# Optimization experiments

Hardware: AMD Instinct MI355X
Metric: run time of the kernel (lower is better)

## Reference

```python
import jax, jax.numpy as jnp
import numpy as np

B, L, V, H = 4096, 80, 256, 512  # batch, NLE_TERM_CO, charset, msg_hdim


def setup_inputs() -> dict:
    key = jax.random.key(0)
    k0, k1, k2 = jax.random.split(key, 3)
    message = jax.random.randint(k0, (B, L), 0, V, dtype=jnp.int64)
    # Linear(i_dim=L*V, H): store weight as [L*V, H] (i.e. torch weight.T)
    W1 = jax.random.normal(k1, (L * V, H), dtype=jnp.float32) * 0.01
    b1 = jnp.zeros((H,), dtype=jnp.float32)
    W2 = jax.random.normal(k2, (H, H), dtype=jnp.float32) * 0.02
    b2 = jnp.zeros((H,), dtype=jnp.float32)
    return {"message": message, "W1": W1, "b1": b1, "W2": W2, "b2": b2}


def reference(message, W1, b1, W2, b2):
    # one_hot(message, 256).reshape(B, L*256) @ W1  ==  gather rows of W1 at
    # flat index pos*256 + char, summed over positions (no one-hot materialized).
    idx = message + jnp.arange(L, dtype=message.dtype)[None, :] * V  # [B, L]
    emb = jnp.take(W1, idx, axis=0).sum(axis=1)                       # [B, H]
    h = jax.nn.relu(emb + b1)
    out = jax.nn.relu(h @ W2 + b2)
    return out
```

## Files before the change

### kernel.cpp

```cpp
#include <hip/hip_runtime.h>
#include <hip/hip_bf16.h>
#include <stdint.h>

#define B_ 4096
#define L_ 80
#define V_ 256
#define H_ 512

typedef __attribute__((ext_vector_type(4))) float f32x4;
typedef __attribute__((ext_vector_type(8))) short bf16x8;

__global__ __launch_bounds__(256) void w2_transpose(
    const float* __restrict__ W2, __hip_bfloat16* __restrict__ W2T) {
  int i = blockIdx.x * blockDim.x + threadIdx.x;
  int n = i >> 9, k = i & 511;
  W2T[i] = __float2bfloat16(W2[k * H_ + n]);
}

__global__ __launch_bounds__(512) void encode_gather(
    const int* __restrict__ msg, const float* __restrict__ W1,
    const float* __restrict__ b1, __hip_bfloat16* __restrict__ h) {
  const int BT = 16;
  __shared__ int offs[BT * L_];
  const int t = threadIdx.x;
  const int b0 = blockIdx.x * BT;

  for (int i = t; i < BT * L_; i += 512) {
    int b = i / L_, l = i - b * L_;
    offs[i] = (l * V_ + msg[(b0 + b) * L_ + l]) * H_;
  }
  __syncthreads();

  float acc[BT];
#pragma unroll
  for (int b = 0; b < BT; ++b) acc[b] = 0.f;

  for (int l = 0; l < L_; ++l) {
#pragma unroll
    for (int b = 0; b < BT; ++b) {
      acc[b] += W1[offs[b * L_ + l] + t];
    }
  }

  const float bias = b1[t];
#pragma unroll
  for (int b = 0; b < BT; ++b) {
    float v = acc[b] + bias;
    v = v > 0.f ? v : 0.f;
    h[(size_t)(b0 + b) * H_ + t] = __float2bfloat16(v);
  }
}

__global__ __launch_bounds__(256) void gemm_out(
    const __hip_bfloat16* __restrict__ h, const __hip_bfloat16* __restrict__ W2T,
    const float* __restrict__ b2, float* __restrict__ out) {
  const int wid = threadIdx.x >> 6;
  const int lane = threadIdx.x & 63;
  const int wm = wid >> 1, wn = wid & 1;
  const int bm = blockIdx.x * 64;
  const int bn = blockIdx.y * 64;
  const int lr = lane & 15;
  const int lq = lane >> 4;

  f32x4 acc[2][2] = {};

  const __hip_bfloat16* aptr0 = h + (size_t)(bm + wm * 32 + lr) * H_ + lq * 8;
  const __hip_bfloat16* bptr0 = W2T + (size_t)(bn + wn * 32 + lr) * H_ + lq * 8;

  for (int kt = 0; kt < H_ / 32; ++kt) {
    const int ko = kt * 32;
    bf16x8 a[2], bfr[2];
#pragma unroll
    for (int mi = 0; mi < 2; ++mi)
      a[mi] = *reinterpret_cast<const bf16x8*>(aptr0 + (size_t)mi * 16 * H_ + ko);
#pragma unroll
    for (int ni = 0; ni < 2; ++ni)
      bfr[ni] = *reinterpret_cast<const bf16x8*>(bptr0 + (size_t)ni * 16 * H_ + ko);
#pragma unroll
    for (int mi = 0; mi < 2; ++mi)
#pragma unroll
      for (int ni = 0; ni < 2; ++ni)
        acc[mi][ni] = __builtin_amdgcn_mfma_f32_16x16x32_bf16(
            a[mi], bfr[ni], acc[mi][ni], 0, 0, 0);
  }

#pragma unroll
  for (int mi = 0; mi < 2; ++mi) {
#pragma unroll
    for (int ni = 0; ni < 2; ++ni) {
      const int n = bn + wn * 32 + ni * 16 + lr;
      const float bias = b2[n];
#pragma unroll
      for (int r = 0; r < 4; ++r) {
        const int m = bm + wm * 32 + mi * 16 + lq * 4 + r;
        float v = acc[mi][ni][r] + bias;
        out[(size_t)m * H_ + n] = v > 0.f ? v : 0.f;
      }
    }
  }
}

extern "C" void kernel_launch(void* const* d_in, const int* in_sizes, int n_in,
                              void* d_out, int out_size, void* d_ws, size_t ws_size,
                              hipStream_t stream) {
  const int* msg   = (const int*)d_in[0];
  const float* W1  = (const float*)d_in[1];
  const float* b1  = (const float*)d_in[2];
  const float* W2  = (const float*)d_in[3];
  const float* b2  = (const float*)d_in[4];
  float* out = (float*)d_out;

  __hip_bfloat16* W2T = (__hip_bfloat16*)d_ws;
  __hip_bfloat16* h   = (__hip_bfloat16*)((char*)d_ws + H_ * H_ * 2);

  hipLaunchKernelGGL(w2_transpose, dim3((H_ * H_) / 256), dim3(256), 0, stream,
                     W2, W2T);
  hipLaunchKernelGGL(encode_gather, dim3(B_ / 16), dim3(512), 0, stream,
                     msg, W1, b1, h);
  hipLaunchKernelGGL(gemm_out, dim3(B_ / 64, H_ / 64), dim3(256), 0, stream,
                     h, W2T, b2, out);
}
```

Before: 149.8 us.

## Convert W1 to bf16 and gather with vectorized wave-uniform row loads

A prep kernel now converts all of W1 to bf16 in workspace and does a shared-memory tiled transpose of W2. The gather kernel then reads bf16 rows with 16-byte vector loads, using readfirstlane so row offsets are wave-uniform, with each wave handling two batch rows. This halves the bytes moved by the dominant random row gathers. In exchange it adds a full pass over the large W1 table on every call and rounds W1 to bf16 before summation. If the workspace is too small, a vectorized fp32 gather is used instead.

```diff
diff --git a/kernel.cpp b/kernel.cpp
--- a/kernel.cpp
+++ b/kernel.cpp
@@ -9,21 +9,56 @@
 
 typedef __attribute__((ext_vector_type(4))) float f32x4;
 typedef __attribute__((ext_vector_type(8))) short bf16x8;
-
-__global__ __launch_bounds__(256) void w2_transpose(
-    const float* __restrict__ W2, __hip_bfloat16* __restrict__ W2T) {
-  int i = blockIdx.x * blockDim.x + threadIdx.x;
-  int n = i >> 9, k = i & 511;
-  W2T[i] = __float2bfloat16(W2[k * H_ + n]);
-}
-
-__global__ __launch_bounds__(512) void encode_gather(
-    const int* __restrict__ msg, const float* __restrict__ W1,
-    const float* __restrict__ b1, __hip_bfloat16* __restrict__ h) {
+typedef __attribute__((ext_vector_type(8))) unsigned short ushort8;
+
+static __device__ __forceinline__ unsigned short f2bf(float x) {
+  union { float f; unsigned int u; } a;
+  a.f = x;
+  unsigned int r = a.u + 0x7fffu + ((a.u >> 16) & 1u);
+  return (unsigned short)(r >> 16);
+}
+static __device__ __forceinline__ float bf2f(unsigned short u) {
+  union { unsigned int i; float f; } a;
+  a.i = ((unsigned int)u) << 16;
+  return a.f;
+}
+
+__global__ __launch_bounds__(256) void prep(
+    const float* __restrict__ W2, const float* __restrict__ W1,
+    unsigned short* __restrict__ W2T, unsigned short* __restrict__ W1b) {
+  const int bid = blockIdx.x;
+  if (bid < 256) {
+    __shared__ float tile[32][33];
+    const int ti = bid & 15, tj = bid >> 4;
+    const int r = threadIdx.x >> 5, c = threadIdx.x & 31;
+#pragma unroll
+    for (int rr = r; rr < 32; rr += 8)
+      tile[rr][c] = W2[(size_t)(ti * 32 + rr) * H_ + tj * 32 + c];
+    __syncthreads();
+#pragma unroll
+    for (int rr = r; rr < 32; rr += 8)
+      W2T[(size_t)(tj * 32 + rr) * H_ + ti * 32 + c] = f2bf(tile[c][rr]);
+  } else {
+    const size_t i8 = ((size_t)(bid - 256) * 256 + threadIdx.x) * 8;
+    f32x4 v0 = *reinterpret_cast<const f32x4*>(W1 + i8);
+    f32x4 v1 = *reinterpret_cast<const f32x4*>(W1 + i8 + 4);
+    ushort8 o;
+    o[0] = f2bf(v0[0]); o[1] = f2bf(v0[1]); o[2] = f2bf(v0[2]); o[3] = f2bf(v0[3]);
+    o[4] = f2bf(v1[0]); o[5] = f2bf(v1[1]); o[6] = f2bf(v1[2]); o[7] = f2bf(v1[3]);
+    *reinterpret_cast<ushort8*>(W1b + i8) = o;
+  }
+}
+
+__global__ __launch_bounds__(512) void encode_gather_bf(
+    const int* __restrict__ msg, const unsigned short* __restrict__ W1b,
+    const float* __restrict__ b1, unsigned short* __restrict__ h) {
   const int BT = 16;
   __shared__ int offs[BT * L_];
   const int t = threadIdx.x;
   const int b0 = blockIdx.x * BT;
+  const int w = t >> 6;
+  const int lane = t & 63;
+  const int c8 = lane * 8;
 
   for (int i = t; i < BT * L_; i += 512) {
     int b = i / L_, l = i - b * L_;
@@ -31,28 +66,74 @@
   }
   __syncthreads();
 
-  float acc[BT];
-#pragma unroll
-  for (int b = 0; b < BT; ++b) acc[b] = 0.f;
-
+  const int r0 = w * 2, r1 = r0 + 1;
+  float a0[8] = {}, a1[8] = {};
+
+#pragma unroll 4
   for (int l = 0; l < L_; ++l) {
-#pragma unroll
-    for (int b = 0; b < BT; ++b) {
-      acc[b] += W1[offs[b * L_ + l] + t];
+    int o0 = __builtin_amdgcn_readfirstlane(offs[r0 * L_ + l]);
+    int o1 = __builtin_amdgcn_readfirstlane(offs[r1 * L_ + l]);
+    ushort8 v0 = *reinterpret_cast<const ushort8*>(W1b + o0 + c8);
+    ushort8 v1 = *reinterpret_cast<const ushort8*>(W1b + o1 + c8);
+#pragma unroll
+    for (int j = 0; j < 8; ++j) {
+      a0[j] += bf2f(v0[j]);
+      a1[j] += bf2f(v1[j]);
     }
   }
 
-  const float bias = b1[t];
-#pragma unroll
-  for (int b = 0; b < BT; ++b) {
-    float v = acc[b] + bias;
-    v = v > 0.f ? v : 0.f;
-    h[(size_t)(b0 + b) * H_ + t] = __float2bfloat16(v);
+  ushort8 o0, o1;
+#pragma unroll
+  for (int j = 0; j < 8; ++j) {
+    float bias = b1[c8 + j];
+    float x0 = a0[j] + bias, x1 = a1[j] + bias;
+    o0[j] = f2bf(x0 > 0.f ? x0 : 0.f);
+    o1[j] = f2bf(x1 > 0.f ? x1 : 0.f);
+  }
+  *reinterpret_cast<ushort8*>(&h[(size_t)(b0 + r0) * H_ + c8]) = o0;
+  *reinterpret_cast<ushort8*>(&h[(size_t)(b0 + r1) * H_ + c8]) = o1;
+}
+
+__global__ __launch_bounds__(512) void encode_gather_f32(
+    const int* __restrict__ msg, const float* __restrict__ W1,
+    const float* __restrict__ b1, unsigned short* __restrict__ h) {
+  const int BT = 16;
+  __shared__ int offs[BT * L_];
+  const int t = threadIdx.x;
+  const int b0 = blockIdx.x * BT;
+  const int g = t >> 7;
+  const int c4 = (t & 127) * 4;
+
+  for (int i = t; i < BT * L_; i += 512) {
+    int b = i / L_, l = i - b * L_;
+    offs[i] = (l * V_ + msg[(b0 + b) * L_ + l]) * H_;
+  }
+  __syncthreads();
+
+  f32x4 acc[4] = {};
+#pragma unroll 2
+  for (int l = 0; l < L_; ++l) {
+#pragma unroll
+    for (int rr = 0; rr < 4; ++rr) {
+      int o = __builtin_amdgcn_readfirstlane(offs[(g * 4 + rr) * L_ + l]);
+      acc[rr] += *reinterpret_cast<const f32x4*>(W1 + o + c4);
+    }
+  }
+  const f32x4 bias = *reinterpret_cast<const f32x4*>(b1 + c4);
+#pragma unroll
+  for (int rr = 0; rr < 4; ++rr) {
+    f32x4 v = acc[rr] + bias;
+    ushort4 o;
+    o.x = f2bf(v[0] > 0.f ? v[0] : 0.f);
+    o.y = f2bf(v[1] > 0.f ? v[1] : 0.f);
+    o.z = f2bf(v[2] > 0.f ? v[2] : 0.f);
+    o.w = f2bf(v[3] > 0.f ? v[3] : 0.f);
+    *reinterpret_cast<ushort4*>(&h[(size_t)(b0 + g * 4 + rr) * H_ + c4]) = o;
   }
 }
 
 __global__ __launch_bounds__(256) void gemm_out(
-    const __hip_bfloat16* __restrict__ h, const __hip_bfloat16* __restrict__ W2T,
+    const unsigned short* __restrict__ h, const unsigned short* __restrict__ W2T,
     const float* __restrict__ b2, float* __restrict__ out) {
   const int wid = threadIdx.x >> 6;
   const int lane = threadIdx.x & 63;
@@ -64,24 +145,25 @@
 
   f32x4 acc[2][2] = {};
 
-  const __hip_bfloat16* aptr0 = h + (size_t)(bm + wm * 32 + lr) * H_ + lq * 8;
-  const __hip_bfloat16* bptr0 = W2T + (size_t)(bn + wn * 32 + lr) * H_ + lq * 8;
-
+  const unsigned short* aptr = h + (size_t)(bm + wm * 32 + lr) * H_ + lq * 8;
+  const unsigned short* bptr = W2T + (size_t)(bn + wn * 32 + lr) * H_ + lq * 8;
+
+#pragma unroll 2
   for (int kt = 0; kt < H_ / 32; ++kt) {
     const int ko = kt * 32;
-    bf16x8 a[2], bfr[2];
+    bf16x8 a[2], bb[2];
 #pragma unroll
     for (int mi = 0; mi < 2; ++mi)
-      a[mi] = *reinterpret_cast<const bf16x8*>(aptr0 + (size_t)mi * 16 * H_ + ko);
+      a[mi] = *reinterpret_cast<const bf16x8*>(aptr + (size_t)mi * 16 * H_ + ko);
 #pragma unroll
     for (int ni = 0; ni < 2; ++ni)
-      bfr[ni] = *reinterpret_cast<const bf16x8*>(bptr0 + (size_t)ni * 16 * H_ + ko);
+      bb[ni] = *reinterpret_cast<const bf16x8*>(bptr + (size_t)ni * 16 * H_ + ko);
 #pragma unroll
     for (int mi = 0; mi < 2; ++mi)
 #pragma unroll
       for (int ni = 0; ni < 2; ++ni)
         acc[mi][ni] = __builtin_amdgcn_mfma_f32_16x16x32_bf16(
-            a[mi], bfr[ni], acc[mi][ni], 0, 0, 0);
+            a[mi], bb[ni], acc[mi][ni], 0, 0, 0);
   }
 
 #pragma unroll
@@ -110,13 +192,29 @@
   const float* b2  = (const float*)d_in[4];
   float* out = (float*)d_out;
 
-  __hip_bfloat16* W2T = (__hip_bfloat16*)d_ws;
-  __hip_bfloat16* h   = (__hip_bfloat16*)((char*)d_ws + H_ * H_ * 2);
-
-  hipLaunchKernelGGL(w2_transpose, dim3((H_ * H_) / 256), dim3(256), 0, stream,
-                     W2, W2T);
-  hipLaunchKernelGGL(encode_gather, dim3(B_ / 16), dim3(512), 0, stream,
-                     msg, W1, b1, h);
+  const size_t W2T_OFF = 0;
+  const size_t H_OFF   = (size_t)H_ * H_ * 2;
+  const size_t W1B_OFF = H_OFF + (size_t)B_ * H_ * 2;
+  const size_t NEED    = W1B_OFF + (size_t)L_ * V_ * H_ * 2;
+
+  unsigned short* W2T = (unsigned short*)((char*)d_ws + W2T_OFF);
+  unsigned short* h   = (unsigned short*)((char*)d_ws + H_OFF);
+  unsigned short* W1b = (unsigned short*)((char*)d_ws + W1B_OFF);
+
+  if (ws_size >= NEED) {
+    const int conv_blocks = (L_ * V_ * H_) / (256 * 8);
+    hipLaunchKernelGGL(prep, dim3(256 + conv_blocks), dim3(256), 0, stream,
+                       W2, W1, W2T, W1b);
+    hipLaunchKernelGGL(encode_gather_bf, dim3(B_ / 16), dim3(512), 0, stream,
+                       msg, W1b, b1, h);
+  } else {
+    const int conv_blocks = 0;
+    hipLaunchKernelGGL(prep, dim3(256 + conv_blocks), dim3(256), 0, stream,
+                       W2, W1, W2T, W1b);
+    hipLaunchKernelGGL(encode_gather_f32, dim3(B_ / 16), dim3(512), 0, stream,
+                       msg, W1, b1, h);
+  }
+
   hipLaunchKernelGGL(gemm_out, dim3(B_ / 64, H_ / 64), dim3(256), 0, stream,
                      h, W2T, b2, out);
 }
```

Result: faster. 140.8 us (-6.0%).
